# Performance work log

Measured on AMD Instinct MI355X. Metric: run time of the kernel, lower is better.

The kernel has to match this reference:

```python
import jax, jax.numpy as jnp
import numpy as np

B, S, D, H, L = 64, 256, 1024, 1024, 2  # input_size == hidden_size required by the module


def _lstm_params(key, in_dim, hid, scale=0.05):
    k1, k2, k3, k4 = jax.random.split(key, 4)
    return (
        jax.random.normal(k1, (4 * hid, in_dim), jnp.float32) * scale,  # W_ih
        jax.random.normal(k2, (4 * hid, hid), jnp.float32) * scale,     # W_hh
        jax.random.normal(k3, (4 * hid,), jnp.float32) * scale,         # b_ih
        jax.random.normal(k4, (4 * hid,), jnp.float32) * scale,         # b_hh
    )


def setup_inputs() -> dict:
    key = jax.random.key(0)
    ks = jax.random.split(key, 5)
    x = jax.random.normal(ks[0], (B, S, D), jnp.float32)
    inp = {"x": x}
    # encoder: LSTM(input_size=D, hidden_size=H, num_layers=L)
    for l, k in enumerate(jax.random.split(ks[1], L)):
        Wih, Whh, bih, bhh = _lstm_params(k, D if l == 0 else H, H)
        inp[f"enc_Wih{l}"], inp[f"enc_Whh{l}"] = Wih, Whh
        inp[f"enc_bih{l}"], inp[f"enc_bhh{l}"] = bih, bhh
    # decoder: LSTM(input_size=H, hidden_size=D, num_layers=L)
    for l, k in enumerate(jax.random.split(ks[2], L)):
        Wih, Whh, bih, bhh = _lstm_params(k, H if l == 0 else D, D)
        inp[f"dec_Wih{l}"], inp[f"dec_Whh{l}"] = Wih, Whh
        inp[f"dec_bih{l}"], inp[f"dec_bhh{l}"] = bih, bhh
    return inp


def _run_lstm(xs, h0, c0, layers):
    """Stacked LSTM over time. xs: [B,S,Din]; h0,c0: [L,B,Hl]. PyTorch gate order i,f,g,o."""
    def step(carry, x_t):
        h, c = carry  # each [L,B,Hl]
        inp = x_t
        new_h, new_c = [], []
        for l, (Wih, Whh, bih, bhh) in enumerate(layers):
            gates = inp @ Wih.T + h[l] @ Whh.T + (bih + bhh)  # [B,4H]
            i, f, g, o = jnp.split(gates, 4, axis=-1)
            c_l = jax.nn.sigmoid(f) * c[l] + jax.nn.sigmoid(i) * jnp.tanh(g)
            h_l = jax.nn.sigmoid(o) * jnp.tanh(c_l)
            new_h.append(h_l)
            new_c.append(c_l)
            inp = h_l
        return (jnp.stack(new_h), jnp.stack(new_c)), inp
    (h_n, c_n), ys = jax.lax.scan(step, (h0, c0), jnp.swapaxes(xs, 0, 1))
    return jnp.swapaxes(ys, 0, 1), h_n, c_n  # ys: [B,S,Hl]


def reference(x,
              enc_Wih0, enc_Whh0, enc_bih0, enc_bhh0,
              enc_Wih1, enc_Whh1, enc_bih1, enc_bhh1,
              dec_Wih0, dec_Whh0, dec_bih0, dec_bhh0,
              dec_Wih1, dec_Whh1, dec_bih1, dec_bhh1):
    enc_layers = [(enc_Wih0, enc_Whh0, enc_bih0, enc_bhh0),
                  (enc_Wih1, enc_Whh1, enc_bih1, enc_bhh1)]
    dec_layers = [(dec_Wih0, dec_Whh0, dec_bih0, dec_bhh0),
                  (dec_Wih1, dec_Whh1, dec_bih1, dec_bhh1)]
    b = x.shape[0]
    z = jnp.zeros((L, b, H), x.dtype)
    # encode
    _, h_n, c_n = _run_lstm(x, z, z, enc_layers)
    emb = h_n[L - 1]  # [B,H]
    # decode: flip feature dim, teacher-forced inputs [emb, flipped_x[:, :-1]]
    flipped_x = jnp.flip(x, axis=2)
    dec_in = jnp.concatenate([emb[:, None, :], flipped_x[:, :-1]], axis=1)  # [B,S,H]
    dec_out, _, _ = _run_lstm(dec_in, h_n, c_n, dec_layers)  # [B,S,D]
    decoded = jnp.flip(dec_out, axis=2)
    return emb, decoded
```

## Files before the change

### kernel.cpp

```cpp
#include <hip/hip_runtime.h>
#include <hip/hip_fp16.h>


#define NBLK 256
#define NTHR 256
#define LDS_BYTES (128 * 1024)
#define HS 65536

typedef _Float16 half8 __attribute__((ext_vector_type(8)));
typedef float    f32x4 __attribute__((ext_vector_type(4)));

__device__ __forceinline__ float sigm_(float x) { return 1.f / (1.f + __expf(-x)); }
__device__ __forceinline__ float tanh_(float x) {
  float e = __expf(-2.f * fabsf(x));
  float r = (1.f - e) / (1.f + e);
  return x >= 0.f ? r : -r;
}

__global__ __launch_bounds__(256) void cvt_x(const float* __restrict__ src,
                                             __half* __restrict__ dst, int n) {
  int i = blockIdx.x * 256 + threadIdx.x;
  if (i < n) dst[i] = __float2half(src[i]);
}

__global__ void fail_mark(float* out, float ws_mb) { out[0] = 1.0e6f * ws_mb; }

__device__ __forceinline__ void issue8c(const __half* p,
    half8& r0, half8& r1, half8& r2, half8& r3,
    half8& r4, half8& r5, half8& r6, half8& r7) {
  asm volatile(
    "global_load_dwordx4 %0, %8, off sc0 sc1\n\t"
    "global_load_dwordx4 %1, %8, off offset:64 sc0 sc1\n\t"
    "global_load_dwordx4 %2, %8, off offset:128 sc0 sc1\n\t"
    "global_load_dwordx4 %3, %8, off offset:192 sc0 sc1\n\t"
    "global_load_dwordx4 %4, %8, off offset:256 sc0 sc1\n\t"
    "global_load_dwordx4 %5, %8, off offset:320 sc0 sc1\n\t"
    "global_load_dwordx4 %6, %8, off offset:384 sc0 sc1\n\t"
    "global_load_dwordx4 %7, %8, off offset:448 sc0 sc1"
    : "=&v"(r0), "=&v"(r1), "=&v"(r2), "=&v"(r3),
      "=&v"(r4), "=&v"(r5), "=&v"(r6), "=&v"(r7)
    : "v"(p) : "memory");
}
__device__ __forceinline__ void issue8p(const __half* p,
    half8& r0, half8& r1, half8& r2, half8& r3,
    half8& r4, half8& r5, half8& r6, half8& r7) {
  asm volatile(
    "global_load_dwordx4 %0, %8, off\n\t"
    "global_load_dwordx4 %1, %8, off offset:64\n\t"
    "global_load_dwordx4 %2, %8, off offset:128\n\t"
    "global_load_dwordx4 %3, %8, off offset:192\n\t"
    "global_load_dwordx4 %4, %8, off offset:256\n\t"
    "global_load_dwordx4 %5, %8, off offset:320\n\t"
    "global_load_dwordx4 %6, %8, off offset:384\n\t"
    "global_load_dwordx4 %7, %8, off offset:448"
    : "=&v"(r0), "=&v"(r1), "=&v"(r2), "=&v"(r3),
      "=&v"(r4), "=&v"(r5), "=&v"(r6), "=&v"(r7)
    : "v"(p) : "memory");
}

__device__ __forceinline__ void st2_coh(__half* p, float h) {
  unsigned v = (unsigned)__half_as_ushort(__float2half(h));
  asm volatile("global_store_short %0, %1, off sc0 sc1" :: "v"(p), "v"(v) : "memory");
}

__device__ __forceinline__ unsigned poll8(const unsigned* c) {
  unsigned a0, a1, a2, a3, a4, a5, a6, a7;
  asm volatile(
    "global_load_dword %0, %8, off sc0 sc1\n\t"
    "global_load_dword %1, %8, off offset:64 sc0 sc1\n\t"
    "global_load_dword %2, %8, off offset:128 sc0 sc1\n\t"
    "global_load_dword %3, %8, off offset:192 sc0 sc1\n\t"
    "global_load_dword %4, %8, off offset:256 sc0 sc1\n\t"
    "global_load_dword %5, %8, off offset:320 sc0 sc1\n\t"
    "global_load_dword %6, %8, off offset:384 sc0 sc1\n\t"
    "global_load_dword %7, %8, off offset:448 sc0 sc1\n\t"
    "s_waitcnt vmcnt(0)"
    : "=&v"(a0), "=&v"(a1), "=&v"(a2), "=&v"(a3),
      "=&v"(a4), "=&v"(a5), "=&v"(a6), "=&v"(a7)
    : "v"(c) : "memory");
  return a0 + a1 + a2 + a3 + a4 + a5 + a6 + a7;
}

#define WAITVM(n) do { asm volatile("s_waitcnt vmcnt(" #n ")" ::: "memory"); \
                       __builtin_amdgcn_sched_barrier(0); } while (0)
#define BANK(X) X##0, X##1, X##2, X##3, X##4, X##5, X##6, X##7
#define ISSUE(X, c) do { const __half* _p = ((c) < 4 ? pa + (c) * 256 : pb + ((c) - 4) * 256); \
                         if (((c) >= 4) && coh1) issue8c(_p, BANK(X)); \
                         else issue8p(_p, BANK(X)); } while (0)
#define MFMA16(X, c) do { const __half* _b = ldsb + (c) * 8192; \
  accA = __builtin_amdgcn_mfma_f32_16x16x32_f16(X##0, *(const half8*)(_b + 0*1024), accA, 0,0,0); \
  accB = __builtin_amdgcn_mfma_f32_16x16x32_f16(X##0, *(const half8*)(_b + 0*1024 + 128), accB, 0,0,0); \
  accA = __builtin_amdgcn_mfma_f32_16x16x32_f16(X##1, *(const half8*)(_b + 1*1024), accA, 0,0,0); \
  accB = __builtin_amdgcn_mfma_f32_16x16x32_f16(X##1, *(const half8*)(_b + 1*1024 + 128), accB, 0,0,0); \
  accA = __builtin_amdgcn_mfma_f32_16x16x32_f16(X##2, *(const half8*)(_b + 2*1024), accA, 0,0,0); \
  accB = __builtin_amdgcn_mfma_f32_16x16x32_f16(X##2, *(const half8*)(_b + 2*1024 + 128), accB, 0,0,0); \
  accA = __builtin_amdgcn_mfma_f32_16x16x32_f16(X##3, *(const half8*)(_b + 3*1024), accA, 0,0,0); \
  accB = __builtin_amdgcn_mfma_f32_16x16x32_f16(X##3, *(const half8*)(_b + 3*1024 + 128), accB, 0,0,0); \
  accA = __builtin_amdgcn_mfma_f32_16x16x32_f16(X##4, *(const half8*)(_b + 4*1024), accA, 0,0,0); \
  accB = __builtin_amdgcn_mfma_f32_16x16x32_f16(X##4, *(const half8*)(_b + 4*1024 + 128), accB, 0,0,0); \
  accA = __builtin_amdgcn_mfma_f32_16x16x32_f16(X##5, *(const half8*)(_b + 5*1024), accA, 0,0,0); \
  accB = __builtin_amdgcn_mfma_f32_16x16x32_f16(X##5, *(const half8*)(_b + 5*1024 + 128), accB, 0,0,0); \
  accA = __builtin_amdgcn_mfma_f32_16x16x32_f16(X##6, *(const half8*)(_b + 6*1024), accA, 0,0,0); \
  accB = __builtin_amdgcn_mfma_f32_16x16x32_f16(X##6, *(const half8*)(_b + 6*1024 + 128), accB, 0,0,0); \
  accA = __builtin_amdgcn_mfma_f32_16x16x32_f16(X##7, *(const half8*)(_b + 7*1024), accA, 0,0,0); \
  accB = __builtin_amdgcn_mfma_f32_16x16x32_f16(X##7, *(const half8*)(_b + 7*1024 + 128), accB, 0,0,0); \
  } while (0)

#define EPI(ACC, CST, BB, NIDX) do { \
  _Pragma("unroll") \
  for (int r = 0; r < 4; ++r) { \
    float v = ACC[r] + (BB); \
    float vx4  = __shfl_xor(v, 4); \
    float vx8  = __shfl_xor(v, 8); \
    float vx12 = __shfl_xor(vx4, 8); \
    float vi = gi == 0 ? v    : gi == 1 ? vx4  : gi == 2 ? vx8  : vx12; \
    float vf = gi == 0 ? vx4  : gi == 1 ? v    : gi == 2 ? vx12 : vx8; \
    float vg = gi == 0 ? vx8  : gi == 1 ? vx12 : gi == 2 ? v    : vx4; \
    float vo = gi == 0 ? vx12 : gi == 1 ? vx8  : gi == 2 ? vx4  : v; \
    float cn = sigm_(vf) * CST[r] + sigm_(vi) * tanh_(vg); \
    CST[r] = cn; \
    float h = sigm_(vo) * tanh_(cn); \
    if (gi == 0) { \
      const int b = mtile * 16 + kq * 4 + r; \
      const int j = jb * 8 + (NIDX) * 4 + (lane & 3); \
      st2_coh(hdst + (size_t)b * 1024 + j, h); \
      if (layer == 1) { \
        if (seg == 0) { if (p == 256) { \
            out[(size_t)b * 1024 + j] = h; \
            st2_coh(femb + (size_t)b * 1024 + (1023 - j), h); } \
        } else { \
          out[65536 + ((size_t)b * 256 + (p - 1)) * 1024 + (1023 - j)] = h; } \
      } \
    } \
  } } while (0)

__global__ __launch_bounds__(256, 1) void lstm_persist(
    const __half* __restrict__ xf16,
    const float* __restrict__ eWih0, const float* __restrict__ eWhh0,
    const float* __restrict__ eWih1, const float* __restrict__ eWhh1,
    const float* __restrict__ dWih0, const float* __restrict__ dWhh0,
    const float* __restrict__ dWih1, const float* __restrict__ dWhh1,
    const float* __restrict__ ebi0, const float* __restrict__ ebh0,
    const float* __restrict__ ebi1, const float* __restrict__ ebh1,
    const float* __restrict__ dbi0, const float* __restrict__ dbh0,
    const float* __restrict__ dbi1, const float* __restrict__ dbh1,
    __half* __restrict__ hE0,
    __half* __restrict__ hD0,
    __half* __restrict__ h1pp,
    __half* __restrict__ femb, float* __restrict__ out,
    unsigned* __restrict__ ctr) {
  extern __shared__ __half lds[];
  const int tid   = threadIdx.x, lane = tid & 63;
  const int mtile = tid >> 6;
  const int layer = blockIdx.x >> 7;
  const int jb    = blockIdx.x & 127;
  const int c4 = lane & 15, kq = lane >> 4;
  const int gi = c4 >> 2;
  const int arow = mtile * 16 + c4;
  unsigned* myctr = ctr + (blockIdx.x & 7) * 16;
  const int coh1 = (layer == 1);

  f32x4 cA = {0.f, 0.f, 0.f, 0.f};
  f32x4 cB = {0.f, 0.f, 0.f, 0.f};
  unsigned tgt = 0;

  for (int seg = 0; seg < 2; ++seg) {
    const float* Wih; const float* Whh; int flip = 0;
    if (seg == 0) { Wih = layer ? eWih1 : eWih0; Whh = layer ? eWhh1 : eWhh0; }
    else { Wih = layer ? dWih1 : dWih0; Whh = layer ? dWhh1 : dWhh0; flip = (layer == 0); }
    const int k0 = tid * 8;
    for (int i = 0; i < 32; ++i) {
      int cc4 = i & 15, ct = i >> 4;
      int n = (cc4 >> 2) * 1024 + jb * 8 + ct * 4 + (cc4 & 3);
      half8 t;
      if (k0 < 1024) {
        if (flip) {
          #pragma unroll
          for (int e = 0; e < 8; ++e) t[e] = (_Float16)Wih[(size_t)n * 1024 + 1023 - k0 - e];
        } else {
          #pragma unroll
          for (int e = 0; e < 8; ++e) t[e] = (_Float16)Wih[(size_t)n * 1024 + k0 + e];
        }
      } else {
        #pragma unroll
        for (int e = 0; e < 8; ++e) t[e] = (_Float16)Whh[(size_t)n * 1024 + k0 - 1024 + e];
      }
      *(half8*)(lds + ((size_t)tid * 32 + i) * 8) = t;
    }
    const float* bi = (seg == 0) ? (layer ? ebi1 : ebi0) : (layer ? dbi1 : dbi0);
    const float* bh = (seg == 0) ? (layer ? ebh1 : ebh0) : (layer ? dbh1 : dbh0);
    const int nl0 = gi * 1024 + jb * 8 + (lane & 3);
    const float bb0 = bi[nl0] + bh[nl0];
    const float bb1 = bi[nl0 + 4] + bh[nl0 + 4];
    __syncthreads();
    asm volatile("s_waitcnt vmcnt(0)" ::: "memory");

    const __half* ldsb = lds + ((size_t)kq * 32 + c4) * 8;
    __half* h0b = seg ? hD0 : hE0;

    for (int p = 0; p <= 256; ++p) {
      const __half* l0rec = (seg && p == 0) ? hE0 + (size_t)256 * HS
                                            : h0b + (size_t)p * HS;
      __half*       l0wr  = h0b + (size_t)(p + 1) * HS;
      const __half* l1in  = h0b + (size_t)p * HS;
      const __half* l1rec = h1pp + (size_t)((p + 1) & 1) * HS;
      __half*       l1wr  = h1pp + (size_t)(p & 1) * HS;

      const int active = (layer == 0) ? (p <= 255) : (p >= 1);
      if (active) {
        const __half* s1 = (layer == 0) ? l0rec : l1rec;
        const __half* s0;
        long long st0;
        if (layer == 0) {
          if (seg == 0)      { s0 = xf16 + (size_t)p * 1024;       st0 = 262144; }
          else if (p == 0)   { s0 = femb;                          st0 = 1024;   }
          else               { s0 = xf16 + (size_t)(p - 1) * 1024; st0 = 262144; }
        } else             { s0 = l1in;                            st0 = 1024;   }

        const __half* pa = s0 + (long long)arow * st0 + kq * 8;
        const __half* pb = s1 + (long long)arow * 1024 + kq * 8;
        f32x4 accA = {0.f, 0.f, 0.f, 0.f};
        f32x4 accB = {0.f, 0.f, 0.f, 0.f};
        half8 A0,A1,A2,A3,A4,A5,A6,A7, B0,B1,B2,B3,B4,B5,B6,B7,
              C0,C1,C2,C3,C4,C5,C6,C7, D0,D1,D2,D3,D4,D5,D6,D7;

        ISSUE(A, 0); ISSUE(B, 1); ISSUE(C, 2); ISSUE(D, 3);
        WAITVM(24); MFMA16(A, 0); ISSUE(A, 4);
        WAITVM(24); MFMA16(B, 1); ISSUE(B, 5);
        WAITVM(24); MFMA16(C, 2); ISSUE(C, 6);
        WAITVM(24); MFMA16(D, 3); ISSUE(D, 7);
        WAITVM(24); MFMA16(A, 4);
        WAITVM(16); MFMA16(B, 5);
        WAITVM(8);  MFMA16(C, 6);
        WAITVM(0);  MFMA16(D, 7);

        __half* hdst = (layer == 0) ? l0wr : l1wr;
        EPI(accA, cA, bb0, 0);
        EPI(accB, cB, bb1, 1);
      }

      tgt += NBLK;
      asm volatile("s_waitcnt vmcnt(0)" ::: "memory");
      __syncthreads();
      if (tid == 0) {
        __hip_atomic_fetch_add(myctr, 1u, __ATOMIC_RELAXED, __HIP_MEMORY_SCOPE_AGENT);
        int guard = 0;
        while (poll8(ctr) < tgt) {
          __builtin_amdgcn_s_sleep(1);
          if (++guard > (1 << 18)) break;
        }
      }
      __syncthreads();
    }
  }
}

extern "C" void kernel_launch(void* const* d_in, const int* in_sizes, int n_in,
                              void* d_out, int out_size, void* d_ws, size_t ws_size,
                              hipStream_t stream) {
  const float* x     = (const float*)d_in[0];
  const float* eWih0 = (const float*)d_in[1];
  const float* eWhh0 = (const float*)d_in[2];
  const float* ebih0 = (const float*)d_in[3];
  const float* ebhh0 = (const float*)d_in[4];
  const float* eWih1 = (const float*)d_in[5];
  const float* eWhh1 = (const float*)d_in[6];
  const float* ebih1 = (const float*)d_in[7];
  const float* ebhh1 = (const float*)d_in[8];
  const float* dWih0 = (const float*)d_in[9];
  const float* dWhh0 = (const float*)d_in[10];
  const float* dbih0 = (const float*)d_in[11];
  const float* dbhh0 = (const float*)d_in[12];
  const float* dWih1 = (const float*)d_in[13];
  const float* dWhh1 = (const float*)d_in[14];
  const float* dbih1 = (const float*)d_in[15];
  const float* dbhh1 = (const float*)d_in[16];
  float* out = (float*)d_out;

  char* ws = (char*)d_ws;
  size_t off = 0;
  auto alloc = [&](size_t bytes) { char* p = ws + off; off += (bytes + 255) & ~(size_t)255; return p; };
  const size_t SLOT = (size_t)HS * sizeof(__half);
  __half* xf16 = (__half*)alloc((size_t)64 * 256 * 1024 * sizeof(__half));
  __half* hE0  = (__half*)alloc(257 * SLOT);
  __half* hD0  = (__half*)alloc(257 * SLOT);
  __half* h1pp = (__half*)alloc(2 * SLOT);
  __half* femb = (__half*)alloc(SLOT);
  unsigned* ctr = (unsigned*)alloc(1024);

  if (ws_size < off) {
    hipLaunchKernelGGL(fail_mark, dim3(1), dim3(1), 0, stream,
                       out, (float)(ws_size >> 20));
    return;
  }

  const int xn = 64 * 256 * 1024;
  cvt_x<<<(xn + 255) / 256, 256, 0, stream>>>(x, xf16, xn);

  hipMemsetAsync(hE0, 0, SLOT, stream);
  hipMemsetAsync(h1pp, 0, SLOT, stream);
  hipMemsetAsync(ctr, 0, 1024, stream);

  hipFuncSetAttribute((const void*)lstm_persist,
                      hipFuncAttributeMaxDynamicSharedMemorySize, LDS_BYTES);
  lstm_persist<<<NBLK, NTHR, LDS_BYTES, stream>>>(
      xf16,
      eWih0, eWhh0, eWih1, eWhh1, dWih0, dWhh0, dWih1, dWhh1,
      ebih0, ebhh0, ebih1, ebhh1, dbih0, dbhh0, dbih1, dbhh1,
      hE0, hD0, h1pp, femb, out, ctr);
}
```

Measured before the change: 6.954 ms.

## Split batch into two pipelined halves with per-wave counter barriers

Blocks drop from four waves to two. Each wave now processes two batch m-tiles in two phases (pipe 0 and pipe 1), and each phase has its own global arrival counter. Waves wait on the other phase's counter instead of doing a block-wide syncthreads plus a single-thread poll. The goal is to overlap one half-batch's barrier latency with the other half's compute, at the cost of serializing the two m-tiles per wave and having every wave poll global counters.

```diff
diff --git a/kernel.cpp b/kernel.cpp
--- a/kernel.cpp
+++ b/kernel.cpp
@@ -3,9 +3,10 @@
 
 
 #define NBLK 256
-#define NTHR 256
+#define NTHR 128
 #define LDS_BYTES (128 * 1024)
 #define HS 65536
+#define ARRV (2 * NBLK)
 
 typedef _Float16 half8 __attribute__((ext_vector_type(8)));
 typedef float    f32x4 __attribute__((ext_vector_type(4)));
@@ -79,6 +80,14 @@
       "=&v"(a4), "=&v"(a5), "=&v"(a6), "=&v"(a7)
     : "v"(c) : "memory");
   return a0 + a1 + a2 + a3 + a4 + a5 + a6 + a7;
+}
+
+__device__ __forceinline__ void wave_wait(const unsigned* c, unsigned tgt) {
+  int guard = 0;
+  while (poll8(c) < tgt) {
+    __builtin_amdgcn_s_sleep(1);
+    if (++guard > (1 << 18)) break;
+  }
 }
 
 #define WAITVM(n) do { asm volatile("s_waitcnt vmcnt(" #n ")" ::: "memory"); \
@@ -134,7 +143,55 @@
     } \
   } } while (0)
 
-__global__ __launch_bounds__(256, 1) void lstm_persist(
+__device__ __forceinline__ void do_phase(
+    int pipe, int p, int seg, int layer, int jb, int wid, int lane,
+    const __half* __restrict__ xf16, const __half* __restrict__ hE0,
+    __half* __restrict__ h0b, __half* __restrict__ h1pp,
+    __half* __restrict__ femb, float* __restrict__ out,
+    const __half* ldsb, float bb0, float bb1, f32x4& cN0, f32x4& cN1) {
+  const int active = (layer == 0) ? (p <= 255) : (p >= 1);
+  if (!active) return;
+  const int c4 = lane & 15, kq = lane >> 4, gi = c4 >> 2;
+  const int mtile = pipe * 2 + wid;
+  const int arow = mtile * 16 + c4;
+  const int coh1 = (layer == 1);
+
+  const __half* l0rec = (seg && p == 0) ? hE0 + (size_t)256 * HS : h0b + (size_t)p * HS;
+  const __half* l1in  = h0b + (size_t)p * HS;
+  const __half* l1rec = h1pp + (size_t)((p + 1) & 1) * HS;
+  const __half* s1 = (layer == 0) ? l0rec : l1rec;
+  const __half* s0;
+  long long st0;
+  if (layer == 0) {
+    if (seg == 0)      { s0 = xf16 + (size_t)p * 1024;       st0 = 262144; }
+    else if (p == 0)   { s0 = femb;                          st0 = 1024;   }
+    else               { s0 = xf16 + (size_t)(p - 1) * 1024; st0 = 262144; }
+  } else             { s0 = l1in;                            st0 = 1024;   }
+
+  const __half* pa = s0 + (long long)arow * st0 + kq * 8;
+  const __half* pb = s1 + (long long)arow * 1024 + kq * 8;
+  f32x4 accA = {0.f, 0.f, 0.f, 0.f};
+  f32x4 accB = {0.f, 0.f, 0.f, 0.f};
+  half8 A0,A1,A2,A3,A4,A5,A6,A7, B0,B1,B2,B3,B4,B5,B6,B7,
+        C0,C1,C2,C3,C4,C5,C6,C7, D0,D1,D2,D3,D4,D5,D6,D7;
+
+  ISSUE(A, 0); ISSUE(B, 1); ISSUE(C, 2); ISSUE(D, 3);
+  WAITVM(24); MFMA16(A, 0); ISSUE(A, 4);
+  WAITVM(24); MFMA16(B, 1); ISSUE(B, 5);
+  WAITVM(24); MFMA16(C, 2); ISSUE(C, 6);
+  WAITVM(24); MFMA16(D, 3); ISSUE(D, 7);
+  WAITVM(24); MFMA16(A, 4);
+  WAITVM(16); MFMA16(B, 5);
+  WAITVM(8);  MFMA16(C, 6);
+  WAITVM(0);  MFMA16(D, 7);
+
+  __half* hdst = (layer == 0) ? h0b + (size_t)(p + 1) * HS
+                              : h1pp + (size_t)(p & 1) * HS;
+  EPI(accA, cN0, bb0, 0);
+  EPI(accB, cN1, bb1, 1);
+}
+
+__global__ __launch_bounds__(128, 1) void lstm_persist(
     const __half* __restrict__ xf16,
     const float* __restrict__ eWih0, const float* __restrict__ eWhh0,
     const float* __restrict__ eWih1, const float* __restrict__ eWhh1,
@@ -144,48 +201,46 @@
     const float* __restrict__ ebi1, const float* __restrict__ ebh1,
     const float* __restrict__ dbi0, const float* __restrict__ dbh0,
     const float* __restrict__ dbi1, const float* __restrict__ dbh1,
-    __half* __restrict__ hE0,
-    __half* __restrict__ hD0,
-    __half* __restrict__ h1pp,
-    __half* __restrict__ femb, float* __restrict__ out,
-    unsigned* __restrict__ ctr) {
+    __half* __restrict__ hE0, __half* __restrict__ hD0,
+    __half* __restrict__ h1pp, __half* __restrict__ femb,
+    float* __restrict__ out, unsigned* __restrict__ ctr) {
   extern __shared__ __half lds[];
-  const int tid   = threadIdx.x, lane = tid & 63;
-  const int mtile = tid >> 6;
+  const int tid  = threadIdx.x, lane = tid & 63, wid = tid >> 6;
   const int layer = blockIdx.x >> 7;
   const int jb    = blockIdx.x & 127;
-  const int c4 = lane & 15, kq = lane >> 4;
-  const int gi = c4 >> 2;
-  const int arow = mtile * 16 + c4;
-  unsigned* myctr = ctr + (blockIdx.x & 7) * 16;
-  const int coh1 = (layer == 1);
-
-  f32x4 cA = {0.f, 0.f, 0.f, 0.f};
-  f32x4 cB = {0.f, 0.f, 0.f, 0.f};
-  unsigned tgt = 0;
+  const int gi = (lane & 15) >> 2;
+  unsigned* ctrA = ctr + (blockIdx.x & 7) * 16;
+  unsigned* ctrB = ctr + 1024 + (blockIdx.x & 7) * 16;
+
+  f32x4 cA0 = {0,0,0,0}, cA1 = {0,0,0,0};
+  f32x4 cB0 = {0,0,0,0}, cB1 = {0,0,0,0};
+  unsigned tgtA = 0, tgtB = 0;
 
   for (int seg = 0; seg < 2; ++seg) {
     const float* Wih; const float* Whh; int flip = 0;
     if (seg == 0) { Wih = layer ? eWih1 : eWih0; Whh = layer ? eWhh1 : eWhh0; }
     else { Wih = layer ? dWih1 : dWih0; Whh = layer ? dWhh1 : dWhh0; flip = (layer == 0); }
-    const int k0 = tid * 8;
-    for (int i = 0; i < 32; ++i) {
-      int cc4 = i & 15, ct = i >> 4;
-      int n = (cc4 >> 2) * 1024 + jb * 8 + ct * 4 + (cc4 & 3);
-      half8 t;
-      if (k0 < 1024) {
-        if (flip) {
-          #pragma unroll
-          for (int e = 0; e < 8; ++e) t[e] = (_Float16)Wih[(size_t)n * 1024 + 1023 - k0 - e];
+    for (int hhalf = 0; hhalf < 2; ++hhalf) {
+      const int t = tid + hhalf * 128;
+      const int k0 = t * 8;
+      for (int i = 0; i < 32; ++i) {
+        int cc4 = i & 15, ct = i >> 4;
+        int n = (cc4 >> 2) * 1024 + jb * 8 + ct * 4 + (cc4 & 3);
+        half8 v;
+        if (k0 < 1024) {
+          if (flip) {
+            #pragma unroll
+            for (int e = 0; e < 8; ++e) v[e] = (_Float16)Wih[(size_t)n * 1024 + 1023 - k0 - e];
+          } else {
+            #pragma unroll
+            for (int e = 0; e < 8; ++e) v[e] = (_Float16)Wih[(size_t)n * 1024 + k0 + e];
+          }
         } else {
           #pragma unroll
-          for (int e = 0; e < 8; ++e) t[e] = (_Float16)Wih[(size_t)n * 1024 + k0 + e];
+          for (int e = 0; e < 8; ++e) v[e] = (_Float16)Whh[(size_t)n * 1024 + k0 - 1024 + e];
         }
-      } else {
-        #pragma unroll
-        for (int e = 0; e < 8; ++e) t[e] = (_Float16)Whh[(size_t)n * 1024 + k0 - 1024 + e];
+        *(half8*)(lds + ((size_t)t * 32 + i) * 8) = v;
       }
-      *(half8*)(lds + ((size_t)tid * 32 + i) * 8) = t;
     }
     const float* bi = (seg == 0) ? (layer ? ebi1 : ebi0) : (layer ? dbi1 : dbi0);
     const float* bh = (seg == 0) ? (layer ? ebh1 : ebh0) : (layer ? dbh1 : dbh0);
@@ -195,63 +250,28 @@
     __syncthreads();
     asm volatile("s_waitcnt vmcnt(0)" ::: "memory");
 
+    const int c4 = lane & 15, kq = lane >> 4;
     const __half* ldsb = lds + ((size_t)kq * 32 + c4) * 8;
     __half* h0b = seg ? hD0 : hE0;
 
     for (int p = 0; p <= 256; ++p) {
-      const __half* l0rec = (seg && p == 0) ? hE0 + (size_t)256 * HS
-                                            : h0b + (size_t)p * HS;
-      __half*       l0wr  = h0b + (size_t)(p + 1) * HS;
-      const __half* l1in  = h0b + (size_t)p * HS;
-      const __half* l1rec = h1pp + (size_t)((p + 1) & 1) * HS;
-      __half*       l1wr  = h1pp + (size_t)(p & 1) * HS;
-
-      const int active = (layer == 0) ? (p <= 255) : (p >= 1);
-      if (active) {
-        const __half* s1 = (layer == 0) ? l0rec : l1rec;
-        const __half* s0;
-        long long st0;
-        if (layer == 0) {
-          if (seg == 0)      { s0 = xf16 + (size_t)p * 1024;       st0 = 262144; }
-          else if (p == 0)   { s0 = femb;                          st0 = 1024;   }
-          else               { s0 = xf16 + (size_t)(p - 1) * 1024; st0 = 262144; }
-        } else             { s0 = l1in;                            st0 = 1024;   }
-
-        const __half* pa = s0 + (long long)arow * st0 + kq * 8;
-        const __half* pb = s1 + (long long)arow * 1024 + kq * 8;
-        f32x4 accA = {0.f, 0.f, 0.f, 0.f};
-        f32x4 accB = {0.f, 0.f, 0.f, 0.f};
-        half8 A0,A1,A2,A3,A4,A5,A6,A7, B0,B1,B2,B3,B4,B5,B6,B7,
-              C0,C1,C2,C3,C4,C5,C6,C7, D0,D1,D2,D3,D4,D5,D6,D7;
-
-        ISSUE(A, 0); ISSUE(B, 1); ISSUE(C, 2); ISSUE(D, 3);
-        WAITVM(24); MFMA16(A, 0); ISSUE(A, 4);
-        WAITVM(24); MFMA16(B, 1); ISSUE(B, 5);
-        WAITVM(24); MFMA16(C, 2); ISSUE(C, 6);
-        WAITVM(24); MFMA16(D, 3); ISSUE(D, 7);
-        WAITVM(24); MFMA16(A, 4);
-        WAITVM(16); MFMA16(B, 5);
-        WAITVM(8);  MFMA16(C, 6);
-        WAITVM(0);  MFMA16(D, 7);
-
-        __half* hdst = (layer == 0) ? l0wr : l1wr;
-        EPI(accA, cA, bb0, 0);
-        EPI(accB, cB, bb1, 1);
-      }
-
-      tgt += NBLK;
+      do_phase(0, p, seg, layer, jb, wid, lane, xf16, hE0, h0b, h1pp, femb, out,
+               ldsb, bb0, bb1, cA0, cA1);
       asm volatile("s_waitcnt vmcnt(0)" ::: "memory");
-      __syncthreads();
-      if (tid == 0) {
-        __hip_atomic_fetch_add(myctr, 1u, __ATOMIC_RELAXED, __HIP_MEMORY_SCOPE_AGENT);
-        int guard = 0;
-        while (poll8(ctr) < tgt) {
-          __builtin_amdgcn_s_sleep(1);
-          if (++guard > (1 << 18)) break;
-        }
-      }
-      __syncthreads();
+      if (lane == 0)
+        __hip_atomic_fetch_add(ctrA, 1u, __ATOMIC_RELAXED, __HIP_MEMORY_SCOPE_AGENT);
+      tgtA += ARRV;
+      wave_wait(ctr + 1024, tgtB);
+      do_phase(1, p, seg, layer, jb, wid, lane, xf16, hE0, h0b, h1pp, femb, out,
+               ldsb, bb0, bb1, cB0, cB1);
+      asm volatile("s_waitcnt vmcnt(0)" ::: "memory");
+      if (lane == 0)
+        __hip_atomic_fetch_add(ctrB, 1u, __ATOMIC_RELAXED, __HIP_MEMORY_SCOPE_AGENT);
+      tgtB += ARRV;
+      wave_wait(ctr, tgtA);
     }
+    wave_wait(ctr + 1024, tgtB);
+    __syncthreads();
   }
 }
 
@@ -286,7 +306,7 @@
   __half* hD0  = (__half*)alloc(257 * SLOT);
   __half* h1pp = (__half*)alloc(2 * SLOT);
   __half* femb = (__half*)alloc(SLOT);
-  unsigned* ctr = (unsigned*)alloc(1024);
+  unsigned* ctr = (unsigned*)alloc(8192);
 
   if (ws_size < off) {
     hipLaunchKernelGGL(fail_mark, dim3(1), dim3(1), 0, stream,
@@ -299,7 +319,7 @@
 
   hipMemsetAsync(hE0, 0, SLOT, stream);
   hipMemsetAsync(h1pp, 0, SLOT, stream);
-  hipMemsetAsync(ctr, 0, 1024, stream);
+  hipMemsetAsync(ctr, 0, 8192, stream);
 
   hipFuncSetAttribute((const void*)lstm_persist,
                       hipFuncAttributeMaxDynamicSharedMemorySize, LDS_BYTES);
```

Result: slower. 7.721 ms (+11.0%).

## Split grid barrier into per-layer counters and prefetch next x tile

Applied to the files above, without the earlier changes.

Replaces the single all-block counter barrier with separate arrival counters for layer-0 and layer-1 blocks. The wait now happens at the start of each step: layer 0 waits only on its own layer, except at the decoder hand-off, while layer 1 waits on both. This lets layer 0 run ahead instead of lock-stepping with layer 1. Layer-0 blocks also prefetch the next step's input-x A-fragments into extra registers before the barrier, so those loads overlap the wait. The cost is higher register pressure from the extra prefetch banks and a more intricate counter-target scheme that must stay correct.

```diff
diff --git a/kernel.cpp b/kernel.cpp
--- a/kernel.cpp
+++ b/kernel.cpp
@@ -63,26 +63,39 @@
   asm volatile("global_store_short %0, %1, off sc0 sc1" :: "v"(p), "v"(v) : "memory");
 }
 
-__device__ __forceinline__ unsigned poll8(const unsigned* c) {
-  unsigned a0, a1, a2, a3, a4, a5, a6, a7;
+__device__ __forceinline__ void poll16(const unsigned* c, unsigned& sA, unsigned& sB) {
+  unsigned a0,a1,a2,a3,a4,a5,a6,a7, b0,b1,b2,b3,b4,b5,b6,b7;
+  const unsigned* c2 = c + 1024;
   asm volatile(
-    "global_load_dword %0, %8, off sc0 sc1\n\t"
-    "global_load_dword %1, %8, off offset:64 sc0 sc1\n\t"
-    "global_load_dword %2, %8, off offset:128 sc0 sc1\n\t"
-    "global_load_dword %3, %8, off offset:192 sc0 sc1\n\t"
-    "global_load_dword %4, %8, off offset:256 sc0 sc1\n\t"
-    "global_load_dword %5, %8, off offset:320 sc0 sc1\n\t"
-    "global_load_dword %6, %8, off offset:384 sc0 sc1\n\t"
-    "global_load_dword %7, %8, off offset:448 sc0 sc1\n\t"
+    "global_load_dword %0, %16, off sc0 sc1\n\t"
+    "global_load_dword %1, %16, off offset:64 sc0 sc1\n\t"
+    "global_load_dword %2, %16, off offset:128 sc0 sc1\n\t"
+    "global_load_dword %3, %16, off offset:192 sc0 sc1\n\t"
+    "global_load_dword %4, %16, off offset:256 sc0 sc1\n\t"
+    "global_load_dword %5, %16, off offset:320 sc0 sc1\n\t"
+    "global_load_dword %6, %16, off offset:384 sc0 sc1\n\t"
+    "global_load_dword %7, %16, off offset:448 sc0 sc1\n\t"
+    "global_load_dword %8, %17, off sc0 sc1\n\t"
+    "global_load_dword %9, %17, off offset:64 sc0 sc1\n\t"
+    "global_load_dword %10, %17, off offset:128 sc0 sc1\n\t"
+    "global_load_dword %11, %17, off offset:192 sc0 sc1\n\t"
+    "global_load_dword %12, %17, off offset:256 sc0 sc1\n\t"
+    "global_load_dword %13, %17, off offset:320 sc0 sc1\n\t"
+    "global_load_dword %14, %17, off offset:384 sc0 sc1\n\t"
+    "global_load_dword %15, %17, off offset:448 sc0 sc1\n\t"
     "s_waitcnt vmcnt(0)"
     : "=&v"(a0), "=&v"(a1), "=&v"(a2), "=&v"(a3),
-      "=&v"(a4), "=&v"(a5), "=&v"(a6), "=&v"(a7)
-    : "v"(c) : "memory");
-  return a0 + a1 + a2 + a3 + a4 + a5 + a6 + a7;
+      "=&v"(a4), "=&v"(a5), "=&v"(a6), "=&v"(a7),
+      "=&v"(b0), "=&v"(b1), "=&v"(b2), "=&v"(b3),
+      "=&v"(b4), "=&v"(b5), "=&v"(b6), "=&v"(b7)
+    : "v"(c), "v"(c2) : "memory");
+  sA = a0 + a1 + a2 + a3 + a4 + a5 + a6 + a7;
+  sB = b0 + b1 + b2 + b3 + b4 + b5 + b6 + b7;
 }
 
 #define WAITVM(n) do { asm volatile("s_waitcnt vmcnt(" #n ")" ::: "memory"); \
                        __builtin_amdgcn_sched_barrier(0); } while (0)
+#define DRAIN()   asm volatile("s_waitcnt vmcnt(0)" ::: "memory")
 #define BANK(X) X##0, X##1, X##2, X##3, X##4, X##5, X##6, X##7
 #define ISSUE(X, c) do { const __half* _p = ((c) < 4 ? pa + (c) * 256 : pb + ((c) - 4) * 256); \
                          if (((c) >= 4) && coh1) issue8c(_p, BANK(X)); \
@@ -105,6 +118,31 @@
   accA = __builtin_amdgcn_mfma_f32_16x16x32_f16(X##7, *(const half8*)(_b + 7*1024), accA, 0,0,0); \
   accB = __builtin_amdgcn_mfma_f32_16x16x32_f16(X##7, *(const half8*)(_b + 7*1024 + 128), accB, 0,0,0); \
   } while (0)
+
+#define PIPE_GENERIC() do { \
+  ISSUE(A, 0); ISSUE(B, 1); ISSUE(C, 2); ISSUE(D, 3); \
+  WAITVM(24); MFMA16(A, 0); ISSUE(A, 4); \
+  WAITVM(24); MFMA16(B, 1); ISSUE(B, 5); \
+  WAITVM(24); MFMA16(C, 2); ISSUE(C, 6); \
+  WAITVM(24); MFMA16(D, 3); ISSUE(D, 7); \
+  WAITVM(24); MFMA16(A, 4); \
+  WAITVM(16); MFMA16(B, 5); \
+  WAITVM(8);  MFMA16(C, 6); \
+  WAITVM(0);  MFMA16(D, 7); \
+} while (0)
+
+#define PIPE_PF() do { \
+  ISSUE(A, 2); ISSUE(B, 3); ISSUE(C, 4); ISSUE(D, 5); \
+  MFMA16(E, 0); MFMA16(F, 1); \
+  WAITVM(24); MFMA16(A, 2); ISSUE(A, 6); \
+  WAITVM(24); MFMA16(B, 3); ISSUE(B, 7); \
+  WAITVM(16); MFMA16(C, 4); \
+  WAITVM(8);  MFMA16(D, 5); \
+  WAITVM(8);  MFMA16(A, 6); \
+  WAITVM(0);  MFMA16(B, 7); \
+} while (0)
+
+#define PREFETCH_EF(ptr) do { issue8p((ptr), BANK(E)); issue8p((ptr) + 256, BANK(F)); } while (0)
 
 #define EPI(ACC, CST, BB, NIDX) do { \
   _Pragma("unroll") \
@@ -157,12 +195,11 @@
   const int c4 = lane & 15, kq = lane >> 4;
   const int gi = c4 >> 2;
   const int arow = mtile * 16 + c4;
-  unsigned* myctr = ctr + (blockIdx.x & 7) * 16;
+  unsigned* myarr = ctr + (layer ? 1024 : 0) + (blockIdx.x & 7) * 16;
   const int coh1 = (layer == 1);
 
   f32x4 cA = {0.f, 0.f, 0.f, 0.f};
   f32x4 cB = {0.f, 0.f, 0.f, 0.f};
-  unsigned tgt = 0;
 
   for (int seg = 0; seg < 2; ++seg) {
     const float* Wih; const float* Whh; int flip = 0;
@@ -193,21 +230,39 @@
     const float bb0 = bi[nl0] + bh[nl0];
     const float bb1 = bi[nl0 + 4] + bh[nl0 + 4];
     __syncthreads();
-    asm volatile("s_waitcnt vmcnt(0)" ::: "memory");
+    DRAIN();
 
     const __half* ldsb = lds + ((size_t)kq * 32 + c4) * 8;
     __half* h0b = seg ? hD0 : hE0;
 
+    half8 A0,A1,A2,A3,A4,A5,A6,A7, B0,B1,B2,B3,B4,B5,B6,B7,
+          C0,C1,C2,C3,C4,C5,C6,C7, D0,D1,D2,D3,D4,D5,D6,D7,
+          E0,E1,E2,E3,E4,E5,E6,E7, F0,F1,F2,F3,F4,F5,F6,F7;
+    int havepf = 0;
+
     for (int p = 0; p <= 256; ++p) {
-      const __half* l0rec = (seg && p == 0) ? hE0 + (size_t)256 * HS
-                                            : h0b + (size_t)p * HS;
-      __half*       l0wr  = h0b + (size_t)(p + 1) * HS;
-      const __half* l1in  = h0b + (size_t)p * HS;
-      const __half* l1rec = h1pp + (size_t)((p + 1) & 1) * HS;
-      __half*       l1wr  = h1pp + (size_t)(p & 1) * HS;
+      const unsigned T  = (unsigned)(seg * 257 + p) * 128u;
+      const unsigned tA = T;
+      const unsigned tB = (layer == 1) ? T
+                         : ((seg == 1 && p == 0) ? 257u * 128u : 0u);
+      if (tid == 0 && (tA | tB)) {
+        unsigned sA, sB;
+        int g = 0;
+        for (;;) {
+          poll16(ctr, sA, sB);
+          if (sA >= tA && sB >= tB) break;
+          __builtin_amdgcn_s_sleep(1);
+          if (++g > (1 << 18)) break;
+        }
+      }
+      __syncthreads();
 
       const int active = (layer == 0) ? (p <= 255) : (p >= 1);
       if (active) {
+        const __half* l0rec = (seg && p == 0) ? hE0 + (size_t)256 * HS
+                                              : h0b + (size_t)p * HS;
+        const __half* l1in  = h0b + (size_t)p * HS;
+        const __half* l1rec = h1pp + (size_t)((p + 1) & 1) * HS;
         const __half* s1 = (layer == 0) ? l0rec : l1rec;
         const __half* s0;
         long long st0;
@@ -221,37 +276,29 @@
         const __half* pb = s1 + (long long)arow * 1024 + kq * 8;
         f32x4 accA = {0.f, 0.f, 0.f, 0.f};
         f32x4 accB = {0.f, 0.f, 0.f, 0.f};
-        half8 A0,A1,A2,A3,A4,A5,A6,A7, B0,B1,B2,B3,B4,B5,B6,B7,
-              C0,C1,C2,C3,C4,C5,C6,C7, D0,D1,D2,D3,D4,D5,D6,D7;
-
-        ISSUE(A, 0); ISSUE(B, 1); ISSUE(C, 2); ISSUE(D, 3);
-        WAITVM(24); MFMA16(A, 0); ISSUE(A, 4);
-        WAITVM(24); MFMA16(B, 1); ISSUE(B, 5);
-        WAITVM(24); MFMA16(C, 2); ISSUE(C, 6);
-        WAITVM(24); MFMA16(D, 3); ISSUE(D, 7);
-        WAITVM(24); MFMA16(A, 4);
-        WAITVM(16); MFMA16(B, 5);
-        WAITVM(8);  MFMA16(C, 6);
-        WAITVM(0);  MFMA16(D, 7);
-
-        __half* hdst = (layer == 0) ? l0wr : l1wr;
+        if (havepf) PIPE_PF(); else PIPE_GENERIC();
+
+        __half* hdst = (layer == 0) ? h0b + (size_t)(p + 1) * HS
+                                    : h1pp + (size_t)(p & 1) * HS;
         EPI(accA, cA, bb0, 0);
         EPI(accB, cB, bb1, 1);
       }
 
-      tgt += NBLK;
-      asm volatile("s_waitcnt vmcnt(0)" ::: "memory");
+      havepf = 0;
+      if (layer == 0 && p < 255) {
+        const __half* ns0 = (seg == 0) ? xf16 + (size_t)(p + 1) * 1024
+                                       : xf16 + (size_t)p * 1024;
+        const __half* npa = ns0 + (long long)arow * 262144 + kq * 8;
+        PREFETCH_EF(npa);
+        havepf = 1;
+      }
+
+      DRAIN();
       __syncthreads();
-      if (tid == 0) {
-        __hip_atomic_fetch_add(myctr, 1u, __ATOMIC_RELAXED, __HIP_MEMORY_SCOPE_AGENT);
-        int guard = 0;
-        while (poll8(ctr) < tgt) {
-          __builtin_amdgcn_s_sleep(1);
-          if (++guard > (1 << 18)) break;
-        }
-      }
-      __syncthreads();
+      if (tid == 0)
+        __hip_atomic_fetch_add(myarr, 1u, __ATOMIC_RELAXED, __HIP_MEMORY_SCOPE_AGENT);
     }
+    __syncthreads();
   }
 }
 
@@ -286,7 +333,7 @@
   __half* hD0  = (__half*)alloc(257 * SLOT);
   __half* h1pp = (__half*)alloc(2 * SLOT);
   __half* femb = (__half*)alloc(SLOT);
-  unsigned* ctr = (unsigned*)alloc(1024);
+  unsigned* ctr = (unsigned*)alloc(8192);
 
   if (ws_size < off) {
     hipLaunchKernelGGL(fail_mark, dim3(1), dim3(1), 0, stream,
@@ -299,7 +346,7 @@
 
   hipMemsetAsync(hE0, 0, SLOT, stream);
   hipMemsetAsync(h1pp, 0, SLOT, stream);
-  hipMemsetAsync(ctr, 0, 1024, stream);
+  hipMemsetAsync(ctr, 0, 8192, stream);
 
   hipFuncSetAttribute((const void*)lstm_persist,
                       hipFuncAttributeMaxDynamicSharedMemorySize, LDS_BYTES);
```

New measurement: 6.748 ms, median of 2. -3.0%, faster.
